# Kernel optimization log

Measured on AMD Instinct MI355X. Metric: run time of the kernel, lower is better.

The kernel has to match this reference:

```python
import jax, jax.numpy as jnp
import numpy as np

D_MODEL = 1024
NHEAD = 16
HEAD_DIM = D_MODEL // NHEAD


def setup_inputs() -> dict:
    key = jax.random.key(0)
    ks = jax.random.split(key, 11)
    B, T = 2, 2048
    s = 1.0 / np.sqrt(D_MODEL)
    return {
        "query": jax.random.normal(ks[0], (B, T, D_MODEL), jnp.float32),
        "key": jax.random.normal(ks[1], (B, T, D_MODEL), jnp.float32),
        "value": jax.random.normal(ks[2], (B, T, D_MODEL), jnp.float32),
        "Wq": jax.random.normal(ks[3], (D_MODEL, D_MODEL), jnp.float32) * s,
        "bq": jnp.zeros((D_MODEL,), jnp.float32),
        "Wk": jax.random.normal(ks[4], (D_MODEL, D_MODEL), jnp.float32) * s,
        "bk": jnp.zeros((D_MODEL,), jnp.float32),
        "Wv": jax.random.normal(ks[5], (D_MODEL, D_MODEL), jnp.float32) * s,
        "bv": jnp.zeros((D_MODEL,), jnp.float32),
        "Wo": jax.random.normal(ks[6], (D_MODEL, D_MODEL), jnp.float32) * s,
        "bo": jnp.zeros((D_MODEL,), jnp.float32),
    }


def reference(query, key, value, Wq, bq, Wk, bk, Wv, bv, Wo, bo):
    B, T, _ = query.shape
    scale = HEAD_DIM ** -0.5
    # Linear projections (torch Linear: x @ W.T + b)
    Q = query @ Wq.T + bq
    K = key @ Wk.T + bk
    V = value @ Wv.T + bv
    # [B, H, T, hd]
    Q = Q.reshape(B, T, NHEAD, HEAD_DIM).transpose(0, 2, 1, 3)
    K = K.reshape(B, T, NHEAD, HEAD_DIM).transpose(0, 2, 1, 3)
    V = V.reshape(B, T, NHEAD, HEAD_DIM).transpose(0, 2, 1, 3)
    # Attention scores [B, H, T, T]
    scores = jnp.einsum("bhqd,bhkd->bhqk", Q, K) * scale
    probs = jax.nn.softmax(scores, axis=-1)
    # dropout is identity in eval mode
    out = jnp.einsum("bhqk,bhkd->bhqd", probs, V)
    out = out.transpose(0, 2, 1, 3).reshape(B, T, D_MODEL)
    return out @ Wo.T + bo
```

## Files before the change

### kernel.cpp

```cpp
#include <hip/hip_runtime.h>
#include <stdint.h>

#define LOG2E_OVER_SQRTHD 0.18033688011112042f
#define SM_BIAS 12.0f

typedef unsigned short u16;
typedef _Float16 f16;
typedef __attribute__((ext_vector_type(4))) float f32x4;
typedef __attribute__((ext_vector_type(16))) float f32x16;
typedef __attribute__((ext_vector_type(8))) _Float16 f16x8;
typedef __attribute__((ext_vector_type(2))) __fp16 fp16x2;

static __device__ __forceinline__ u16 f2h_bits(float f) {
  union { f16 h; u16 u; } v; v.h = (f16)f; return v.u;
}
static __device__ __forceinline__ uint32_t pkrtz(float a, float b) {
  union { fp16x2 h; uint32_t u; } v;
  v.h = __builtin_amdgcn_cvt_pkrtz(a, b);
  return v.u;
}

static __device__ __forceinline__ void g2l16(const void* g, void* l) {
  __builtin_amdgcn_global_load_lds((const __attribute__((address_space(1))) void*)g,
                                   (__attribute__((address_space(3))) void*)l,
                                   16, 0, 0);
}

__global__ __launch_bounds__(256) void pack_all(
    const float* __restrict__ q, const float* __restrict__ k, const float* __restrict__ v,
    const float* __restrict__ wq, const float* __restrict__ wk,
    const float* __restrict__ wv, const float* __restrict__ wo,
    u16* __restrict__ X, u16* __restrict__ W) {
  int flat = blockIdx.x * 256 + threadIdx.x;
  const float* src;
  u16* dst;
  int idx;
  if (flat < 3 * 1048576) {
    int z = flat >> 20;
    idx = flat & 1048575;
    src = (z == 0) ? q : (z == 1) ? k : v;
    dst = X + (size_t)z * 4194304;
  } else {
    int f2 = flat - 3 * 1048576;
    int z = f2 >> 18;
    idx = f2 & 262143;
    src = (z == 0) ? wq : (z == 1) ? wk : (z == 2) ? wv : wo;
    dst = W + (size_t)z * 1048576;
  }
  float4 x = ((const float4*)src)[idx];
  ushort4 o;
  o.x = f2h_bits(x.x); o.y = f2h_bits(x.y); o.z = f2h_bits(x.z); o.w = f2h_bits(x.w);
  *(ushort4*)(dst + (size_t)idx * 4) = o;
}

template <bool OUT_F16>
static __device__ __forceinline__ void gemm_body(
    const u16* __restrict__ A, const u16* __restrict__ W,
    const float* __restrict__ bias, void* __restrict__ C,
    int ldc, bool row_bias, float oscale, int bm, int bn) {
  __shared__ u16 As[2][128 * 32];
  __shared__ u16 Bs[2][128 * 32];
  const int tid = threadIdx.x;
  const int lane = tid & 63;
  const int wave = tid >> 6;
  const int wm = wave >> 1, wn = wave & 1;
  const int quad = lane >> 4, l15 = lane & 15;

  f32x4 acc[4][4] = {};

  const int r0 = tid >> 2;
  const int c0 = (tid & 3) * 8;
  const u16* Ab = A + (size_t)bm * 1024 + (size_t)r0 * 1024 + c0;
  const u16* Wb = W + (size_t)bn * 1024 + (size_t)r0 * 1024 + c0;

  g2l16(Ab, As[0] + tid * 8);
  g2l16(Ab + 64 * 1024, As[0] + (256 + tid) * 8);
  g2l16(Wb, Bs[0] + tid * 8);
  g2l16(Wb + 64 * 1024, Bs[0] + (256 + tid) * 8);
  __syncthreads();

  for (int kt = 0; kt < 32; ++kt) {
    const int p = kt & 1;
    if (kt + 1 < 32) {
      const int kc = (kt + 1) * 32;
      g2l16(Ab + kc, As[p ^ 1] + tid * 8);
      g2l16(Ab + 64 * 1024 + kc, As[p ^ 1] + (256 + tid) * 8);
      g2l16(Wb + kc, Bs[p ^ 1] + tid * 8);
      g2l16(Wb + 64 * 1024 + kc, Bs[p ^ 1] + (256 + tid) * 8);
    }
    f16x8 af[4], bw[4];
#pragma unroll
    for (int mt = 0; mt < 4; ++mt)
      af[mt] = *(const f16x8*)(As[p] + (wm * 64 + mt * 16 + l15) * 32 + quad * 8);
#pragma unroll
    for (int nt = 0; nt < 4; ++nt)
      bw[nt] = *(const f16x8*)(Bs[p] + (wn * 64 + nt * 16 + l15) * 32 + quad * 8);
#pragma unroll
    for (int mt = 0; mt < 4; ++mt)
#pragma unroll
      for (int nt = 0; nt < 4; ++nt)
        acc[mt][nt] = __builtin_amdgcn_mfma_f32_16x16x32_f16(af[mt], bw[nt], acc[mt][nt], 0, 0, 0);
    __syncthreads();
  }

#pragma unroll
  for (int mt = 0; mt < 4; ++mt) {
    const int row = bm + wm * 64 + mt * 16 + quad * 4;
#pragma unroll
    for (int nt = 0; nt < 4; ++nt) {
      const int col = bn + wn * 64 + nt * 16 + l15;
      const float bcol = row_bias ? 0.0f : bias[col];
#pragma unroll
      for (int i = 0; i < 4; ++i) {
        const float bb = row_bias ? bias[row + i] : bcol;
        float val = (acc[mt][nt][i] + bb) * oscale;
        if (OUT_F16)
          ((u16*)C)[(size_t)(row + i) * ldc + col] = f2h_bits(val);
        else
          ((float*)C)[(size_t)(row + i) * ldc + col] = val;
      }
    }
  }
}

__global__ __launch_bounds__(256) void gemm_qkv(const u16* __restrict__ X,
    const u16* __restrict__ Wf, const float* __restrict__ bq,
    const float* __restrict__ bk, const float* __restrict__ bv,
    u16* __restrict__ QK, u16* __restrict__ Vt, float qscale) {
  const int z = blockIdx.z;
  if (z == 0) {
    gemm_body<true>(X, Wf, bq, QK, 1024, false, qscale,
                    blockIdx.x * 128, blockIdx.y * 128);
  } else if (z == 1) {
    gemm_body<true>(X + (size_t)4194304, Wf + (size_t)1048576, bk,
                    QK + (size_t)4194304, 1024, false, 1.0f,
                    blockIdx.x * 128, blockIdx.y * 128);
  } else {
    gemm_body<true>(Wf + (size_t)2 * 1048576, X + (size_t)2 * 4194304, bv,
                    Vt, 4096, true, 1.0f,
                    blockIdx.y * 128, blockIdx.x * 128);
  }
}

__global__ __launch_bounds__(256) void gemm_out(const u16* __restrict__ O,
    const u16* __restrict__ Wo, const float* __restrict__ bo,
    float* __restrict__ out) {
  gemm_body<false>(O, Wo, bo, out, 1024, false, 1.0f,
                   blockIdx.x * 128, blockIdx.y * 128);
}

__global__ __launch_bounds__(512, 4) void attn_kernel(const u16* __restrict__ QK,
                                                      const u16* __restrict__ Vt,
                                                      u16* __restrict__ O) {
  __shared__ u16 lds[40960];
  u16* Qs = lds;

  const u16* Qb = QK;
  const u16* Kb = QK + (size_t)4096 * 1024;

  const int tid = threadIdx.x, lane = tid & 63, wave = tid >> 6;
  const int q31 = lane & 31, hh = lane >> 5;
  const int set = wave >> 2, w4 = wave & 3;

  const int id = blockIdx.x;
  const int xcd = id & 7;
  const int j = id >> 3;
  const int qt = j & 15;
  const int hb = xcd + 8 * (j >> 4);
  const int h = hb & 15, b = hb >> 4;

  const size_t qrow0 = (size_t)b * 2048 + qt * 128;
  const size_t kv0 = (size_t)b * 2048;
  const int hc = h * 64;

  const int rq = tid >> 3;
  const int pq = tid & 7;
  const int sq = (pq ^ (rq & 7)) * 8;
  g2l16(Qb + (qrow0 + rq) * 1024 + hc + sq, Qs + tid * 8);
  g2l16(Qb + (qrow0 + 64 + rq) * 1024 + hc + sq, Qs + (512 + tid) * 8);

  const int st = tid & 255;
  const int r0 = st >> 3;
  const int p0 = st & 7;
  const int s0 = (p0 ^ (r0 & 7)) * 8;

  const int kt0 = set * 16;
  u16* KsS  = lds + 8192  + set * 8192;
  u16* VtsS = lds + 24576 + set * 8192;

  {
    const size_t kr = kv0 + (size_t)kt0 * 64;
    g2l16(Kb + (kr + r0) * 1024 + hc + s0, KsS + st * 8);
    g2l16(Kb + (kr + 32 + r0) * 1024 + hc + s0, KsS + (256 + st) * 8);
    g2l16(Vt + (size_t)(hc + r0) * 4096 + kr + s0, VtsS + st * 8);
    g2l16(Vt + (size_t)(hc + 32 + r0) * 4096 + kr + s0, VtsS + (256 + st) * 8);
  }
  __syncthreads();

  f16x8 qf[4];
  const int Rq = w4 * 32 + q31;
#pragma unroll
  for (int c = 0; c < 4; ++c)
    qf[c] = *(const f16x8*)(Qs + Rq * 64 + (((2 * c + hh) ^ (Rq & 7)) * 8));

  f32x16 oacc[2] = {};
  float l_lane = 0.f;

  for (int it = 0; it < 16; ++it) {
    const int p = it & 1;
    if (it + 1 < 16) {
      const size_t kr1 = kv0 + (size_t)(kt0 + it + 1) * 64;
      u16* Kd = KsS + (p ^ 1) * 4096;
      u16* Vd = VtsS + (p ^ 1) * 4096;
      g2l16(Kb + (kr1 + r0) * 1024 + hc + s0, Kd + st * 8);
      g2l16(Kb + (kr1 + 32 + r0) * 1024 + hc + s0, Kd + (256 + st) * 8);
      g2l16(Vt + (size_t)(hc + r0) * 4096 + kr1 + s0, Vd + st * 8);
      g2l16(Vt + (size_t)(hc + 32 + r0) * 4096 + kr1 + s0, Vd + (256 + st) * 8);
    }
    const u16* Kc = KsS + p * 4096;
    const u16* Vc = VtsS + p * 4096;

    f32x16 sac[2];
#pragma unroll
    for (int t = 0; t < 2; ++t)
#pragma unroll
      for (int r = 0; r < 16; ++r) sac[t][r] = -SM_BIAS;
#pragma unroll
    for (int t = 0; t < 2; ++t) {
      const int Rk = t * 32 + q31;
#pragma unroll
      for (int c = 0; c < 4; ++c) {
        f16x8 kf = *(const f16x8*)(Kc + Rk * 64 + (((2 * c + hh) ^ (Rk & 7)) * 8));
        sac[t] = __builtin_amdgcn_mfma_f32_32x32x16_f16(kf, qf[c], sac[t], 0, 0, 0);
      }
    }

    uint32_t dd[2][8];
#pragma unroll
    for (int t = 0; t < 2; ++t) {
      float pe[16];
#pragma unroll
      for (int r = 0; r < 16; ++r) pe[r] = __builtin_amdgcn_exp2f(sac[t][r]);
      float a0 = (pe[0] + pe[1]) + (pe[2] + pe[3]);
      float a1 = (pe[4] + pe[5]) + (pe[6] + pe[7]);
      float a2 = (pe[8] + pe[9]) + (pe[10] + pe[11]);
      float a3 = (pe[12] + pe[13]) + (pe[14] + pe[15]);
      l_lane += (a0 + a1) + (a2 + a3);
#pragma unroll
      for (int k = 0; k < 8; ++k) dd[t][k] = pkrtz(pe[2 * k], pe[2 * k + 1]);
    }

    uint32_t rp[2][4];
#pragma unroll
    for (int t = 0; t < 2; ++t) {
      uint32_t y0 = hh ? dd[t][0] : dd[t][2];
      uint32_t y1 = hh ? dd[t][1] : dd[t][3];
      uint32_t y2 = hh ? dd[t][4] : dd[t][6];
      uint32_t y3 = hh ? dd[t][5] : dd[t][7];
      rp[t][0] = (uint32_t)__shfl_xor((int)y0, 32);
      rp[t][1] = (uint32_t)__shfl_xor((int)y1, 32);
      rp[t][2] = (uint32_t)__shfl_xor((int)y2, 32);
      rp[t][3] = (uint32_t)__shfl_xor((int)y3, 32);
    }

    f16x8 pf[4];
#pragma unroll
    for (int t = 0; t < 2; ++t)
#pragma unroll
      for (int u = 0; u < 2; ++u) {
        union { uint32_t w[4]; f16x8 v; } fr;
        fr.w[0] = hh ? rp[t][2 * u]     : dd[t][4 * u];
        fr.w[1] = hh ? rp[t][2 * u + 1] : dd[t][4 * u + 1];
        fr.w[2] = hh ? dd[t][4 * u + 2] : rp[t][2 * u];
        fr.w[3] = hh ? dd[t][4 * u + 3] : rp[t][2 * u + 1];
        pf[2 * t + u] = fr.v;
      }

#pragma unroll
    for (int dt2 = 0; dt2 < 2; ++dt2) {
      const int Rv = dt2 * 32 + q31;
#pragma unroll
      for (int ch = 0; ch < 4; ++ch) {
        f16x8 vf = *(const f16x8*)(Vc + Rv * 64 + (((2 * ch + hh) ^ (Rv & 7)) * 8));
        oacc[dt2] = __builtin_amdgcn_mfma_f32_32x32x16_f16(vf, pf[ch], oacc[dt2], 0, 0, 0);
      }
    }

    __syncthreads();
  }

  const float l_set = l_lane + __shfl_xor(l_lane, 32);

  float* Of = (float*)(lds + 24576);
  float* Ll = (float*)lds;
  u16* bounce = lds + 8192;
  const int orow = w4 * 32 + q31;

  if (set == 1) {
#pragma unroll
    for (int dt2 = 0; dt2 < 2; ++dt2)
#pragma unroll
      for (int r = 0; r < 16; ++r) {
        const int d = dt2 * 32 + (r & 3) + 8 * (r >> 2) + 4 * hh;
        Of[d * 128 + orow] = oacc[dt2][r];
      }
    if (hh == 0) Ll[orow] = l_set;
  }
  __syncthreads();

  if (set == 0) {
    const float inv = 1.0f / (l_set + Ll[orow]);
#pragma unroll
    for (int dt2 = 0; dt2 < 2; ++dt2)
#pragma unroll
      for (int w = 0; w < 8; ++w) {
        const int dbase = dt2 * 32 + 4 * hh + 8 * (w >> 1) + 2 * (w & 1);
        float va = (oacc[dt2][2 * w]     + Of[dbase * 128 + orow]) * inv;
        float vb = (oacc[dt2][2 * w + 1] + Of[(dbase + 1) * 128 + orow]) * inv;
        uint32_t pk2 = (uint32_t)f2h_bits(va) | ((uint32_t)f2h_bits(vb) << 16);
        *(uint32_t*)(bounce + orow * 72 + dbase) = pk2;
      }
  }
  __syncthreads();

  const int row2 = tid >> 2, q2 = tid & 3;
#pragma unroll
  for (int k = 0; k < 2; ++k) {
    const int chunk = q2 + 4 * k;
    uint4 v4 = *(const uint4*)(bounce + row2 * 72 + chunk * 8);
    *(uint4*)(O + (qrow0 + row2) * 1024 + hc + chunk * 8) = v4;
  }
}

extern "C" void kernel_launch(void* const* d_in, const int* in_sizes, int n_in,
                              void* d_out, int out_size, void* d_ws, size_t ws_size,
                              hipStream_t stream) {
  const float* query = (const float*)d_in[0];
  const float* key   = (const float*)d_in[1];
  const float* value = (const float*)d_in[2];
  const float* Wq = (const float*)d_in[3];
  const float* bq = (const float*)d_in[4];
  const float* Wk = (const float*)d_in[5];
  const float* bk = (const float*)d_in[6];
  const float* Wv = (const float*)d_in[7];
  const float* bv = (const float*)d_in[8];
  const float* Wo = (const float*)d_in[9];
  const float* bo = (const float*)d_in[10];
  float* out = (float*)d_out;

  u16* X  = (u16*)d_ws;
  u16* W  = X + (size_t)3 * 4194304;
  u16* QK = W + (size_t)4 * 1048576;
  u16* Vt = QK + (size_t)2 * 4194304;
  u16* O  = X;

  pack_all<<<dim3(16384, 1, 1), 256, 0, stream>>>(query, key, value, Wq, Wk, Wv, Wo, X, W);
  gemm_qkv<<<dim3(32, 8, 3), 256, 0, stream>>>(X, W, bq, bk, bv, QK, Vt,
                                               LOG2E_OVER_SQRTHD);
  attn_kernel<<<dim3(512, 1, 1), 512, 0, stream>>>(QK, Vt, O);
  gemm_out<<<dim3(32, 8, 1), 256, 0, stream>>>(O, W + (size_t)3 * 1048576, bo, out);
}
```

Measured before the change: 233.3 us.

## Split-K output projection with atomic accumulation and MFMA priority hints in attention

The output projection GEMM is split four ways along K, with each split adding its partial tile into a zeroed float output through atomicAdd. Only the first split adds the bias. This raises the grid from 256 to 1024 blocks to better fill the GPU's compute units. It costs an extra memset plus atomic read-modify-write traffic on the output. The attention kernel also wraps its MFMA sections in s_setprio(1)/s_setprio(0) so waves issuing matrix ops are favoured by the scheduler.

```diff
diff --git a/kernel.cpp b/kernel.cpp
--- a/kernel.cpp
+++ b/kernel.cpp
@@ -53,11 +53,12 @@
   *(ushort4*)(dst + (size_t)idx * 4) = o;
 }
 
-template <bool OUT_F16>
+template <bool OUT_F16, bool ATOMIC = false>
 static __device__ __forceinline__ void gemm_body(
     const u16* __restrict__ A, const u16* __restrict__ W,
     const float* __restrict__ bias, void* __restrict__ C,
-    int ldc, bool row_bias, float oscale, int bm, int bn) {
+    int ldc, bool row_bias, float oscale, int bm, int bn,
+    int kt0, int nkt) {
   __shared__ u16 As[2][128 * 32];
   __shared__ u16 Bs[2][128 * 32];
   const int tid = threadIdx.x;
@@ -70,8 +71,9 @@
 
   const int r0 = tid >> 2;
   const int c0 = (tid & 3) * 8;
-  const u16* Ab = A + (size_t)bm * 1024 + (size_t)r0 * 1024 + c0;
-  const u16* Wb = W + (size_t)bn * 1024 + (size_t)r0 * 1024 + c0;
+  const int kbase = kt0 * 32;
+  const u16* Ab = A + (size_t)bm * 1024 + (size_t)r0 * 1024 + c0 + kbase;
+  const u16* Wb = W + (size_t)bn * 1024 + (size_t)r0 * 1024 + c0 + kbase;
 
   g2l16(Ab, As[0] + tid * 8);
   g2l16(Ab + 64 * 1024, As[0] + (256 + tid) * 8);
@@ -79,9 +81,9 @@
   g2l16(Wb + 64 * 1024, Bs[0] + (256 + tid) * 8);
   __syncthreads();
 
-  for (int kt = 0; kt < 32; ++kt) {
+  for (int kt = 0; kt < nkt; ++kt) {
     const int p = kt & 1;
-    if (kt + 1 < 32) {
+    if (kt + 1 < nkt) {
       const int kc = (kt + 1) * 32;
       g2l16(Ab + kc, As[p ^ 1] + tid * 8);
       g2l16(Ab + 64 * 1024 + kc, As[p ^ 1] + (256 + tid) * 8);
@@ -109,12 +111,14 @@
 #pragma unroll
     for (int nt = 0; nt < 4; ++nt) {
       const int col = bn + wn * 64 + nt * 16 + l15;
-      const float bcol = row_bias ? 0.0f : bias[col];
+      const float bcol = (row_bias || !bias) ? 0.0f : bias[col];
 #pragma unroll
       for (int i = 0; i < 4; ++i) {
         const float bb = row_bias ? bias[row + i] : bcol;
         float val = (acc[mt][nt][i] + bb) * oscale;
-        if (OUT_F16)
+        if (ATOMIC)
+          atomicAdd(&((float*)C)[(size_t)(row + i) * ldc + col], val);
+        else if (OUT_F16)
           ((u16*)C)[(size_t)(row + i) * ldc + col] = f2h_bits(val);
         else
           ((float*)C)[(size_t)(row + i) * ldc + col] = val;
@@ -130,23 +134,24 @@
   const int z = blockIdx.z;
   if (z == 0) {
     gemm_body<true>(X, Wf, bq, QK, 1024, false, qscale,
-                    blockIdx.x * 128, blockIdx.y * 128);
+                    blockIdx.x * 128, blockIdx.y * 128, 0, 32);
   } else if (z == 1) {
     gemm_body<true>(X + (size_t)4194304, Wf + (size_t)1048576, bk,
                     QK + (size_t)4194304, 1024, false, 1.0f,
-                    blockIdx.x * 128, blockIdx.y * 128);
+                    blockIdx.x * 128, blockIdx.y * 128, 0, 32);
   } else {
     gemm_body<true>(Wf + (size_t)2 * 1048576, X + (size_t)2 * 4194304, bv,
                     Vt, 4096, true, 1.0f,
-                    blockIdx.y * 128, blockIdx.x * 128);
-  }
-}
-
-__global__ __launch_bounds__(256) void gemm_out(const u16* __restrict__ O,
+                    blockIdx.y * 128, blockIdx.x * 128, 0, 32);
+  }
+}
+
+__global__ __launch_bounds__(256) void gemm_out_splitk(const u16* __restrict__ O,
     const u16* __restrict__ Wo, const float* __restrict__ bo,
     float* __restrict__ out) {
-  gemm_body<false>(O, Wo, bo, out, 1024, false, 1.0f,
-                   blockIdx.x * 128, blockIdx.y * 128);
+  const int z = blockIdx.z;
+  gemm_body<false, true>(O, Wo, (z == 0) ? bo : nullptr, out, 1024, false, 1.0f,
+                         blockIdx.x * 128, blockIdx.y * 128, z * 8, 8);
 }
 
 __global__ __launch_bounds__(512, 4) void attn_kernel(const u16* __restrict__ QK,
@@ -225,6 +230,7 @@
     for (int t = 0; t < 2; ++t)
 #pragma unroll
       for (int r = 0; r < 16; ++r) sac[t][r] = -SM_BIAS;
+    __builtin_amdgcn_s_setprio(1);
 #pragma unroll
     for (int t = 0; t < 2; ++t) {
       const int Rk = t * 32 + q31;
@@ -234,6 +240,7 @@
         sac[t] = __builtin_amdgcn_mfma_f32_32x32x16_f16(kf, qf[c], sac[t], 0, 0, 0);
       }
     }
+    __builtin_amdgcn_s_setprio(0);
 
     uint32_t dd[2][8];
 #pragma unroll
@@ -276,6 +283,7 @@
         pf[2 * t + u] = fr.v;
       }
 
+    __builtin_amdgcn_s_setprio(1);
 #pragma unroll
     for (int dt2 = 0; dt2 < 2; ++dt2) {
       const int Rv = dt2 * 32 + q31;
@@ -285,6 +293,7 @@
         oacc[dt2] = __builtin_amdgcn_mfma_f32_32x32x16_f16(vf, pf[ch], oacc[dt2], 0, 0, 0);
       }
     }
+    __builtin_amdgcn_s_setprio(0);
 
     __syncthreads();
   }
@@ -358,5 +367,6 @@
   gemm_qkv<<<dim3(32, 8, 3), 256, 0, stream>>>(X, W, bq, bk, bv, QK, Vt,
                                                LOG2E_OVER_SQRTHD);
   attn_kernel<<<dim3(512, 1, 1), 512, 0, stream>>>(QK, Vt, O);
-  gemm_out<<<dim3(32, 8, 1), 256, 0, stream>>>(O, W + (size_t)3 * 1048576, bo, out);
-}
+  hipMemsetAsync(out, 0, (size_t)4096 * 1024 * sizeof(float), stream);
+  gemm_out_splitk<<<dim3(32, 8, 4), 256, 0, stream>>>(O, W + (size_t)3 * 1048576, bo, out);
+}
```

Result: slower. 266.7 us (+14.3%).

## Use 64x64-tile output GEMM and raise wave priority around attention MFMAs

Applied to the files above, without the earlier changes.

Replaces the 128x128-tiled output projection with a dedicated 64x64-tile kernel on 16x16x32 MFMAs. This launches 1024 blocks instead of 256, so the 256 compute units of the MI355X are better filled. The attention loop also wraps its two MFMA phases in s_setprio so that matrix work is issued ahead of the exp and shuffle work from other waves. The smaller tiles lower data reuse and add global and LDS traffic per FLOP, and the new LDS layout is unswizzled, which may cause bank conflicts.

```diff
diff --git a/kernel.cpp b/kernel.cpp
--- a/kernel.cpp
+++ b/kernel.cpp
@@ -142,11 +142,63 @@
   }
 }
 
-__global__ __launch_bounds__(256) void gemm_out(const u16* __restrict__ O,
+__global__ __launch_bounds__(256) void gemm_out64(const u16* __restrict__ O,
     const u16* __restrict__ Wo, const float* __restrict__ bo,
     float* __restrict__ out) {
-  gemm_body<false>(O, Wo, bo, out, 1024, false, 1.0f,
-                   blockIdx.x * 128, blockIdx.y * 128);
+  __shared__ u16 As[2][64 * 32];
+  __shared__ u16 Bs[2][64 * 32];
+  const int tid = threadIdx.x;
+  const int lane = tid & 63;
+  const int wave = tid >> 6;
+  const int wm = wave >> 1, wn = wave & 1;
+  const int quad = lane >> 4, l15 = lane & 15;
+  const int bm = blockIdx.x * 64, bn = blockIdx.y * 64;
+
+  f32x4 acc[2][2] = {};
+
+  const int r0 = tid >> 2;
+  const int c0 = (tid & 3) * 8;
+  const u16* Ab = O + (size_t)(bm + r0) * 1024 + c0;
+  const u16* Wb = Wo + (size_t)(bn + r0) * 1024 + c0;
+
+  g2l16(Ab, As[0] + tid * 8);
+  g2l16(Wb, Bs[0] + tid * 8);
+  __syncthreads();
+
+  for (int kt = 0; kt < 32; ++kt) {
+    const int p = kt & 1;
+    if (kt + 1 < 32) {
+      const int kc = (kt + 1) * 32;
+      g2l16(Ab + kc, As[p ^ 1] + tid * 8);
+      g2l16(Wb + kc, Bs[p ^ 1] + tid * 8);
+    }
+    f16x8 af[2], bw[2];
+#pragma unroll
+    for (int mt = 0; mt < 2; ++mt)
+      af[mt] = *(const f16x8*)(As[p] + (wm * 32 + mt * 16 + l15) * 32 + quad * 8);
+#pragma unroll
+    for (int nt = 0; nt < 2; ++nt)
+      bw[nt] = *(const f16x8*)(Bs[p] + (wn * 32 + nt * 16 + l15) * 32 + quad * 8);
+#pragma unroll
+    for (int mt = 0; mt < 2; ++mt)
+#pragma unroll
+      for (int nt = 0; nt < 2; ++nt)
+        acc[mt][nt] = __builtin_amdgcn_mfma_f32_16x16x32_f16(af[mt], bw[nt], acc[mt][nt], 0, 0, 0);
+    __syncthreads();
+  }
+
+#pragma unroll
+  for (int mt = 0; mt < 2; ++mt) {
+    const int row = bm + wm * 32 + mt * 16 + quad * 4;
+#pragma unroll
+    for (int nt = 0; nt < 2; ++nt) {
+      const int col = bn + wn * 32 + nt * 16 + l15;
+      const float bcol = bo[col];
+#pragma unroll
+      for (int i = 0; i < 4; ++i)
+        out[(size_t)(row + i) * 1024 + col] = acc[mt][nt][i] + bcol;
+    }
+  }
 }
 
 __global__ __launch_bounds__(512, 4) void attn_kernel(const u16* __restrict__ QK,
@@ -225,6 +277,7 @@
     for (int t = 0; t < 2; ++t)
 #pragma unroll
       for (int r = 0; r < 16; ++r) sac[t][r] = -SM_BIAS;
+    __builtin_amdgcn_s_setprio(1);
 #pragma unroll
     for (int t = 0; t < 2; ++t) {
       const int Rk = t * 32 + q31;
@@ -234,6 +287,7 @@
         sac[t] = __builtin_amdgcn_mfma_f32_32x32x16_f16(kf, qf[c], sac[t], 0, 0, 0);
       }
     }
+    __builtin_amdgcn_s_setprio(0);
 
     uint32_t dd[2][8];
 #pragma unroll
@@ -276,6 +330,7 @@
         pf[2 * t + u] = fr.v;
       }
 
+    __builtin_amdgcn_s_setprio(1);
 #pragma unroll
     for (int dt2 = 0; dt2 < 2; ++dt2) {
       const int Rv = dt2 * 32 + q31;
@@ -285,6 +340,7 @@
         oacc[dt2] = __builtin_amdgcn_mfma_f32_32x32x16_f16(vf, pf[ch], oacc[dt2], 0, 0, 0);
       }
     }
+    __builtin_amdgcn_s_setprio(0);
 
     __syncthreads();
   }
@@ -358,5 +414,5 @@
   gemm_qkv<<<dim3(32, 8, 3), 256, 0, stream>>>(X, W, bq, bk, bv, QK, Vt,
                                                LOG2E_OVER_SQRTHD);
   attn_kernel<<<dim3(512, 1, 1), 512, 0, stream>>>(QK, Vt, O);
-  gemm_out<<<dim3(32, 8, 1), 256, 0, stream>>>(O, W + (size_t)3 * 1048576, bo, out);
-}
+  gemm_out64<<<dim3(64, 16, 1), 256, 0, stream>>>(O, W + (size_t)3 * 1048576, bo, out);
+}
```

Result: faster. 226.1 us (-3.1%).
